# Kernel tuning notes

Hardware: AMD Instinct MI355X
Metric: run time of the kernel (lower is better)

Reference implementation:

```python
import jax, jax.numpy as jnp
import numpy as np


def _rotate_half(t):
    h = t.shape[-1] // 2
    return jnp.concatenate([-t[..., h:], t[..., :h]], axis=-1)


def setup_inputs() -> dict:
    key = jax.random.key(0)
    ks = jax.random.split(key, 4)
    B, S, H, NH, NKV, HD, MT = 1, 2048, 4096, 32, 8, 128, 8192
    x = jax.random.normal(ks[0], (B, S, H), jnp.float32)
    # real RoPE tables (HF rotate_half convention): [S, head_dim]
    inv_freq = 1.0 / (10000.0 ** (jnp.arange(0, HD, 2, dtype=jnp.float32) / HD))
    freqs = jnp.arange(S, dtype=jnp.float32)[:, None] * inv_freq[None, :]
    emb = jnp.concatenate([freqs, freqs], axis=-1)
    cos, sin = jnp.cos(emb), jnp.sin(emb)
    wq = jax.random.normal(ks[1], (H, H), jnp.float32) * 0.02
    w_kv = jax.random.normal(ks[2], (2 * NKV * HD, H), jnp.float32) * 0.02
    wo = jax.random.normal(ks[3], (H, H), jnp.float32) * 0.02
    cur_select_index = jnp.arange(B * S, dtype=jnp.int32)  # token slots in cache
    kv_buffer = jnp.zeros((MT, 2 * NKV, HD), jnp.float32)
    return dict(x=x, cos=cos, sin=sin, wq=wq, w_kv=w_kv, wo=wo,
                cur_select_index=cur_select_index, kv_buffer=kv_buffer)


def reference(x, cos, sin, wq, w_kv, wo, cur_select_index, kv_buffer):
    B, S, H = x.shape
    HD = cos.shape[-1]
    NKV = w_kv.shape[0] // (2 * HD)
    NH = H // HD
    # fused QKV projections
    q = (x @ wq.T).reshape(B, S, NH, HD)
    kvp = x @ w_kv.T  # [B, S, 2*NKV*HD]
    k = kvp[..., : NKV * HD].reshape(B, S, NKV, HD)
    v = kvp[..., NKV * HD:].reshape(B, S, NKV, HD)
    # RoPE (rotate_half), cos/sin broadcast over batch and heads
    c = cos[None, :, None, :]
    s = sin[None, :, None, :]
    q = q * c + _rotate_half(q) * s
    k = k * c + _rotate_half(k) * s
    # scatter KV-cache update: [B*S, 2*NKV, HD] into flat token cache
    combined_kv = jnp.concatenate([k, v], axis=2).reshape(B * S, 2 * NKV, HD)
    kv_new = kv_buffer.at[cur_select_index].set(combined_kv)
    # GQA: replicate kv heads to match query heads
    rep = NH // NKV
    kr = jnp.repeat(k, rep, axis=2)  # [B, S, NH, HD]
    vr = jnp.repeat(v, rep, axis=2)
    scale = 1.0 / jnp.sqrt(jnp.float32(HD))
    scores = jnp.einsum('bqhd,bkhd->bhqk', q, kr) * scale  # [B, NH, S, S]
    causal = jnp.tril(jnp.ones((S, S), dtype=bool))
    scores = jnp.where(causal[None, None], scores, jnp.float32(-1e9))
    p = jax.nn.softmax(scores, axis=-1)
    attn = jnp.einsum('bhqk,bkhd->bqhd', p, vr).reshape(B, S, H)
    out = attn @ wo.T
    return out, kv_new
```

## Files before the change

### kernel.cpp

```cpp
#include <hip/hip_runtime.h>
#include <stdint.h>
#include <stddef.h>

typedef __attribute__((ext_vector_type(8))) short bf16x8;
typedef __attribute__((ext_vector_type(4))) float f32x4;
typedef unsigned short u16;
typedef unsigned int u32;

static __device__ __forceinline__ u16 f2bf(float f) {
    u32 u = __builtin_bit_cast(u32, f);
    u = u + 0x7FFFu + ((u >> 16) & 1u);
    return (u16)(u >> 16);
}
static __device__ __forceinline__ float bf2f(u16 h) {
    return __builtin_bit_cast(float, (u32)h << 16);
}

typedef const __attribute__((address_space(1))) u32* gas1_t;
typedef __attribute__((address_space(3))) u32* las3_t;
static __device__ __forceinline__ void gload_lds16(const void* g, void* l) {
    __builtin_amdgcn_global_load_lds((gas1_t)g, (las3_t)l, 16, 0, 0);
}

__global__ __launch_bounds__(256) void k_cvt(const float* __restrict__ s,
                                             u16* __restrict__ d, int n) {
    int i = (blockIdx.x * 256 + threadIdx.x) * 4;
    if (i >= n) return;
    float4 f = *(const float4*)(s + i);
    ushort4 o;
    o.x = f2bf(f.x); o.y = f2bf(f.y); o.z = f2bf(f.z); o.w = f2bf(f.w);
    *(ushort4*)(d + i) = o;
}

template <bool F32OUT>
__global__ __launch_bounds__(256) void k_gemm_bt(const u16* __restrict__ A,
                                                 const u16* __restrict__ B,
                                                 void* __restrict__ Cv,
                                                 int M, int N, int K) {
    __shared__ alignas(16) unsigned char sA[16384];
    __shared__ alignas(16) unsigned char sB[16384];
    const int tid = threadIdx.x;
    const int lane = tid & 63;
    const int wid = tid >> 6;
    const int l15 = lane & 15, l4 = lane >> 4;
    const int brow = blockIdx.y * 128;
    const int bcol = blockIdx.x * 128;
    const int wr = wid >> 1, wc = wid & 1;

    f32x4 acc[4][4];
#pragma unroll
    for (int m = 0; m < 4; ++m)
#pragma unroll
        for (int n = 0; n < 4; ++n) acc[m][n] = (f32x4){0.f, 0.f, 0.f, 0.f};

    const int pbase = wid * 4096 + lane * 16;
    const int nk = K >> 6;
    for (int kt = 0; kt < nk; ++kt) {
        __syncthreads();
#pragma unroll
        for (int i = 0; i < 4; ++i) {
            const int p = pbase + i * 1024;
            const int row = p >> 7;
            const int colb = (p & 127) ^ ((row & 7) << 4);
            const char* gA = (const char*)(A + (size_t)(brow + row) * K + (kt << 6)) + colb;
            const char* gB = (const char*)(B + (size_t)(bcol + row) * K + (kt << 6)) + colb;
            gload_lds16(gA, sA + wid * 4096 + i * 1024);
            gload_lds16(gB, sB + wid * 4096 + i * 1024);
        }
        __syncthreads();
#pragma unroll
        for (int kk = 0; kk < 2; ++kk) {
            bf16x8 af[4], bfr[4];
#pragma unroll
            for (int m = 0; m < 4; ++m) {
                const int row = wr * 64 + m * 16 + l15;
                const int colb = (kk * 64 + l4 * 16) ^ ((row & 7) << 4);
                af[m] = *(const bf16x8*)(sA + row * 128 + colb);
            }
#pragma unroll
            for (int n = 0; n < 4; ++n) {
                const int row = wc * 64 + n * 16 + l15;
                const int colb = (kk * 64 + l4 * 16) ^ ((row & 7) << 4);
                bfr[n] = *(const bf16x8*)(sB + row * 128 + colb);
            }
#pragma unroll
            for (int m = 0; m < 4; ++m)
#pragma unroll
                for (int n = 0; n < 4; ++n)
                    acc[m][n] = __builtin_amdgcn_mfma_f32_16x16x32_bf16(
                        af[m], bfr[n], acc[m][n], 0, 0, 0);
        }
    }
#pragma unroll
    for (int m = 0; m < 4; ++m)
#pragma unroll
        for (int n = 0; n < 4; ++n)
#pragma unroll
            for (int q = 0; q < 4; ++q) {
                const int row = brow + wr * 64 + m * 16 + l4 * 4 + q;
                const int col = bcol + wc * 64 + n * 16 + l15;
                if constexpr (F32OUT)
                    ((float*)Cv)[(size_t)row * N + col] = acc[m][n][q];
                else
                    ((u16*)Cv)[(size_t)row * N + col] = f2bf(acc[m][n][q]);
            }
}

__global__ __launch_bounds__(256) void k_rope(u16* __restrict__ q,
                                              u16* __restrict__ kv,
                                              const float* __restrict__ cosb,
                                              const float* __restrict__ sinb) {
    int i = blockIdx.x * 256 + threadIdx.x;
    int s = i / 2560;
    int rem = i - s * 2560;
    int hh = rem >> 6;
    int d = rem & 63;
    float c = cosb[s * 128 + d];
    float sn = sinb[s * 128 + d];
    u16* p = (hh < 32) ? (q + (size_t)s * 4096 + hh * 128 + d)
                       : (kv + (size_t)s * 2048 + (hh - 32) * 128 + d);
    float a = bf2f(p[0]);
    float b = bf2f(p[64]);
    p[0]  = f2bf(a * c - b * sn);
    p[64] = f2bf(b * c + a * sn);
}

__global__ __launch_bounds__(256) void k_scatter(const u16* __restrict__ kv,
                                                 const int* __restrict__ sel,
                                                 float* __restrict__ kvnew) {
    int i = blockIdx.x * 256 + threadIdx.x;
    int row = i >> 9;
    int c4 = (i & 511) << 2;
    int r = sel[row];
    ushort4 v = *(const ushort4*)(kv + (size_t)row * 2048 + c4);
    float4 f;
    f.x = bf2f(v.x); f.y = bf2f(v.y); f.z = bf2f(v.z); f.w = bf2f(v.w);
    *(float4*)(kvnew + (size_t)r * 2048 + c4) = f;
}

__global__ __launch_bounds__(256) void k_attn(const u16* __restrict__ Q,
                                              const u16* __restrict__ KV,
                                              u16* __restrict__ Oa, int S) {
    __shared__ alignas(16) unsigned char sQ[16384];
    __shared__ alignas(16) unsigned char sK[16384];
    __shared__ alignas(16) unsigned char sV[16384];
    __shared__ alignas(16) unsigned char sP[4 * 16 * 160];
    const int tid = threadIdx.x;
    const int lane = tid & 63;
    const int w = tid >> 6;
    const int l15 = lane & 15, l4 = lane >> 4;
    const int h = blockIdx.x;
    const int q0 = blockIdx.y * 64;
    const int hk = h >> 2;

    {
        const int pb = w * 4096 + lane * 16;
#pragma unroll
        for (int i = 0; i < 4; ++i) {
            const int p = pb + i * 1024;
            const int row = p >> 8;
            const int colb = (p & 255) ^ ((row & 7) << 4);
            const char* g = (const char*)(Q + (size_t)(q0 + row) * 4096 + h * 128) + colb;
            gload_lds16(g, sQ + w * 4096 + i * 1024);
        }
    }
    __syncthreads();
    bf16x8 qf[4];
    {
        const int row = w * 16 + l15;
#pragma unroll
        for (int kk = 0; kk < 4; ++kk) {
            const int colb = (kk * 64 + l4 * 16) ^ ((row & 7) << 4);
            qf[kk] = *(const bf16x8*)(sQ + row * 256 + colb);
        }
    }
    float mrow[4] = {-1e30f, -1e30f, -1e30f, -1e30f};
    float lrow[4] = {0.f, 0.f, 0.f, 0.f};
    f32x4 oacc[8];
#pragma unroll
    for (int dn = 0; dn < 8; ++dn) oacc[dn] = (f32x4){0.f, 0.f, 0.f, 0.f};

    const float scale = 0.08838834764831845f;
    const int ntiles = (q0 >> 6) + 1;
    for (int t = 0; t < ntiles; ++t) {
        const int kv0 = t << 6;
        __syncthreads();
        {
            const int pb = w * 4096 + lane * 16;
#pragma unroll
            for (int i = 0; i < 4; ++i) {
                const int p = pb + i * 1024;
                const int row = p >> 8;
                const int colb = (p & 255) ^ ((row & 7) << 4);
                const char* gk = (const char*)(KV + (size_t)(kv0 + row) * 2048 + hk * 128) + colb;
                const char* gv = (const char*)(KV + (size_t)(kv0 + row) * 2048 + 1024 + hk * 128) + colb;
                gload_lds16(gk, sK + w * 4096 + i * 1024);
                gload_lds16(gv, sV + w * 4096 + i * 1024);
            }
        }
        __syncthreads();
        f32x4 sf[4];
#pragma unroll
        for (int n = 0; n < 4; ++n) {
            sf[n] = (f32x4){0.f, 0.f, 0.f, 0.f};
#pragma unroll
            for (int kk = 0; kk < 4; ++kk) {
                const int row = n * 16 + l15;
                const int colb = (kk * 64 + l4 * 16) ^ ((row & 7) << 4);
                bf16x8 kf = *(const bf16x8*)(sK + row * 256 + colb);
                sf[n] = __builtin_amdgcn_mfma_f32_16x16x32_bf16(qf[kk], kf, sf[n], 0, 0, 0);
            }
        }
        const bool diag = (kv0 == q0);
#pragma unroll
        for (int n = 0; n < 4; ++n)
#pragma unroll
            for (int q = 0; q < 4; ++q) {
                float v = sf[n][q] * scale;
                if (diag) {
                    const int col = n * 16 + l15;
                    const int rowq = w * 16 + l4 * 4 + q;
                    if (col > rowq) v = -1e9f;
                }
                sf[n][q] = v;
            }
        float al[4], rsum[4];
#pragma unroll
        for (int q = 0; q < 4; ++q) {
            float m0 = fmaxf(fmaxf(sf[0][q], sf[1][q]), fmaxf(sf[2][q], sf[3][q]));
#pragma unroll
            for (int d = 1; d < 16; d <<= 1) m0 = fmaxf(m0, __shfl_xor(m0, d));
            const float mn = fmaxf(mrow[q], m0);
            al[q] = __expf(mrow[q] - mn);
            mrow[q] = mn;
            rsum[q] = 0.f;
        }
#pragma unroll
        for (int n = 0; n < 4; ++n)
#pragma unroll
            for (int q = 0; q < 4; ++q) {
                float p = __expf(sf[n][q] - mrow[q]);
                sf[n][q] = p;
                rsum[q] += p;
            }
#pragma unroll
        for (int q = 0; q < 4; ++q) {
#pragma unroll
            for (int d = 1; d < 16; d <<= 1) rsum[q] += __shfl_xor(rsum[q], d);
            lrow[q] = lrow[q] * al[q] + rsum[q];
        }
#pragma unroll
        for (int dn = 0; dn < 8; ++dn) {
            oacc[dn][0] *= al[0]; oacc[dn][1] *= al[1];
            oacc[dn][2] *= al[2]; oacc[dn][3] *= al[3];
        }
        {
            u16* pw = (u16*)(sP + w * 2560);
#pragma unroll
            for (int n = 0; n < 4; ++n)
#pragma unroll
                for (int q = 0; q < 4; ++q)
                    pw[(l4 * 4 + q) * 80 + n * 16 + l15] = f2bf(sf[n][q]);
        }
#pragma unroll
        for (int kk2 = 0; kk2 < 2; ++kk2) {
            bf16x8 pf = *(const bf16x8*)(sP + w * 2560 + l15 * 160 + kk2 * 64 + l4 * 16);
#pragma unroll
            for (int dn = 0; dn < 8; ++dn) {
                bf16x8 vf;
#pragma unroll
                for (int j = 0; j < 8; ++j) {
                    const int k = kk2 * 32 + l4 * 8 + j;
                    const int byteoff = k * 256 + ((dn * 32 + l15 * 2) ^ ((k & 7) << 4));
                    vf[j] = (short)*(const u16*)(sV + byteoff);
                }
                oacc[dn] = __builtin_amdgcn_mfma_f32_16x16x32_bf16(pf, vf, oacc[dn], 0, 0, 0);
            }
        }
    }
#pragma unroll
    for (int dn = 0; dn < 8; ++dn)
#pragma unroll
        for (int q = 0; q < 4; ++q) {
            const int row = q0 + w * 16 + l4 * 4 + q;
            const int col = h * 128 + dn * 16 + l15;
            Oa[(size_t)row * 4096 + col] = f2bf(oacc[dn][q] / lrow[q]);
        }
}

extern "C" void kernel_launch(void* const* d_in, const int* in_sizes, int n_in,
                              void* d_out, int out_size, void* d_ws, size_t ws_size,
                              hipStream_t stream) {
    (void)n_in; (void)out_size; (void)ws_size;
    const float* x    = (const float*)d_in[0];
    const float* cosb = (const float*)d_in[1];
    const float* sinb = (const float*)d_in[2];
    const float* wq   = (const float*)d_in[3];
    const float* wkv  = (const float*)d_in[4];
    const float* wo   = (const float*)d_in[5];
    const int*   sel  = (const int*)d_in[6];
    const float* kvbuf = (const float*)d_in[7];

    const int H = 4096, HKV = 2048;
    const int S = in_sizes[0] / H;
    const int MT = in_sizes[7] / HKV;

    char* ws = (char*)d_ws;
    u16* xb    = (u16*)(ws);
    u16* attnb = (u16*)(ws);
    u16* wqb   = (u16*)(ws + (16u << 20));
    u16* wob   = (u16*)(ws + (16u << 20));
    u16* wkvb  = (u16*)(ws + (48u << 20));
    u16* qb    = (u16*)(ws + (64u << 20));
    u16* kvb   = (u16*)(ws + (80u << 20));

    float* out = (float*)d_out;
    float* kvnew = out + (size_t)S * H;

    const int nx = S * H, nwq = H * H, nwkv = HKV * H, nwo = H * H;
    k_cvt<<<nx / 1024, 256, 0, stream>>>(x, xb, nx);
    k_cvt<<<nwq / 1024, 256, 0, stream>>>(wq, wqb, nwq);
    k_cvt<<<nwkv / 1024, 256, 0, stream>>>(wkv, wkvb, nwkv);

    k_gemm_bt<false><<<dim3(H / 128, S / 128), 256, 0, stream>>>(xb, wqb, qb, S, H, H);
    k_gemm_bt<false><<<dim3(HKV / 128, S / 128), 256, 0, stream>>>(xb, wkvb, kvb, S, HKV, H);

    k_cvt<<<nwo / 1024, 256, 0, stream>>>(wo, wob, nwo);

    k_rope<<<(S * 2560) / 256, 256, 0, stream>>>(qb, kvb, cosb, sinb);

    hipMemcpyAsync(kvnew, kvbuf, (size_t)MT * HKV * sizeof(float),
                   hipMemcpyDeviceToDevice, stream);
    k_scatter<<<(S * HKV / 4) / 256, 256, 0, stream>>>(kvb, sel, kvnew);

    k_attn<<<dim3(32, S / 64), 256, 0, stream>>>(qb, kvb, attnb, S);

    k_gemm_bt<true><<<dim3(H / 128, S / 128), 256, 0, stream>>>(attnb, wob, out, S, H, H);
}
```

Measured before the change: 716.2 us.

## Transpose V into LDS through registers for vectorized PV operand reads

V tiles are now loaded into registers, transposed with 16-bit pack/shift operations, and stored to LDS in a d-major swizzled layout. The PV MFMA B operand then comes from a single 16-byte LDS read instead of eight scalar u16 reads. The P staging buffer now reuses the Q shared buffer, since Q lives in registers after the prologue. The cost is that V no longer uses async direct-to-LDS loads: it takes synchronous global loads plus register shuffling each tile, which can stall before the barrier.

```diff
diff --git a/kernel.cpp b/kernel.cpp
--- a/kernel.cpp
+++ b/kernel.cpp
@@ -141,10 +141,9 @@
 __global__ __launch_bounds__(256) void k_attn(const u16* __restrict__ Q,
                                               const u16* __restrict__ KV,
                                               u16* __restrict__ Oa, int S) {
-    __shared__ alignas(16) unsigned char sQ[16384];
+    __shared__ alignas(16) unsigned char sQP[16384];
     __shared__ alignas(16) unsigned char sK[16384];
     __shared__ alignas(16) unsigned char sV[16384];
-    __shared__ alignas(16) unsigned char sP[4 * 16 * 160];
     const int tid = threadIdx.x;
     const int lane = tid & 63;
     const int w = tid >> 6;
@@ -161,7 +160,7 @@
             const int row = p >> 8;
             const int colb = (p & 255) ^ ((row & 7) << 4);
             const char* g = (const char*)(Q + (size_t)(q0 + row) * 4096 + h * 128) + colb;
-            gload_lds16(g, sQ + w * 4096 + i * 1024);
+            gload_lds16(g, sQP + w * 4096 + i * 1024);
         }
     }
     __syncthreads();
@@ -171,7 +170,7 @@
 #pragma unroll
         for (int kk = 0; kk < 4; ++kk) {
             const int colb = (kk * 64 + l4 * 16) ^ ((row & 7) << 4);
-            qf[kk] = *(const bf16x8*)(sQ + row * 256 + colb);
+            qf[kk] = *(const bf16x8*)(sQP + row * 256 + colb);
         }
     }
     float mrow[4] = {-1e30f, -1e30f, -1e30f, -1e30f};
@@ -179,12 +178,23 @@
     f32x4 oacc[8];
 #pragma unroll
     for (int dn = 0; dn < 8; ++dn) oacc[dn] = (f32x4){0.f, 0.f, 0.f, 0.f};
+
+    const int vko = (tid & 7) * 8;
+    const int vdq = (tid >> 3) * 4;
 
     const float scale = 0.08838834764831845f;
     const int ntiles = (q0 >> 6) + 1;
     for (int t = 0; t < ntiles; ++t) {
         const int kv0 = t << 6;
         __syncthreads();
+        u32 vin[8][2];
+#pragma unroll
+        for (int i = 0; i < 8; ++i) {
+            const u32* g = (const u32*)(KV + (size_t)(kv0 + vko + i) * 2048 +
+                                        1024 + hk * 128 + vdq);
+            vin[i][0] = g[0];
+            vin[i][1] = g[1];
+        }
         {
             const int pb = w * 4096 + lane * 16;
 #pragma unroll
@@ -193,10 +203,33 @@
                 const int row = p >> 8;
                 const int colb = (p & 255) ^ ((row & 7) << 4);
                 const char* gk = (const char*)(KV + (size_t)(kv0 + row) * 2048 + hk * 128) + colb;
-                const char* gv = (const char*)(KV + (size_t)(kv0 + row) * 2048 + 1024 + hk * 128) + colb;
                 gload_lds16(gk, sK + w * 4096 + i * 1024);
-                gload_lds16(gv, sV + w * 4096 + i * 1024);
-            }
+            }
+        }
+#pragma unroll
+        for (int q = 0; q < 4; ++q) {
+            const int d = vdq + q;
+            uint4 ow;
+            {
+                const int wsel = q >> 1;
+                u32 a0 = vin[0][wsel], b0 = vin[1][wsel];
+                u32 a1 = vin[2][wsel], b1 = vin[3][wsel];
+                u32 a2 = vin[4][wsel], b2 = vin[5][wsel];
+                u32 a3 = vin[6][wsel], b3 = vin[7][wsel];
+                if (q & 1) {
+                    ow.x = (a0 >> 16) | (b0 & 0xFFFF0000u);
+                    ow.y = (a1 >> 16) | (b1 & 0xFFFF0000u);
+                    ow.z = (a2 >> 16) | (b2 & 0xFFFF0000u);
+                    ow.w = (a3 >> 16) | (b3 & 0xFFFF0000u);
+                } else {
+                    ow.x = (a0 & 0xFFFFu) | (b0 << 16);
+                    ow.y = (a1 & 0xFFFFu) | (b1 << 16);
+                    ow.z = (a2 & 0xFFFFu) | (b2 << 16);
+                    ow.w = (a3 & 0xFFFFu) | (b3 << 16);
+                }
+            }
+            const int byteoff = d * 128 + ((vko * 2) ^ ((d & 7) << 4));
+            *(uint4*)(sV + byteoff) = ow;
         }
         __syncthreads();
         f32x4 sf[4];
@@ -255,7 +288,7 @@
             oacc[dn][2] *= al[2]; oacc[dn][3] *= al[3];
         }
         {
-            u16* pw = (u16*)(sP + w * 2560);
+            u16* pw = (u16*)(sQP + w * 2560);
 #pragma unroll
             for (int n = 0; n < 4; ++n)
 #pragma unroll
@@ -264,16 +297,12 @@
         }
 #pragma unroll
         for (int kk2 = 0; kk2 < 2; ++kk2) {
-            bf16x8 pf = *(const bf16x8*)(sP + w * 2560 + l15 * 160 + kk2 * 64 + l4 * 16);
+            bf16x8 pf = *(const bf16x8*)(sQP + w * 2560 + l15 * 160 + kk2 * 64 + l4 * 16);
 #pragma unroll
             for (int dn = 0; dn < 8; ++dn) {
-                bf16x8 vf;
-#pragma unroll
-                for (int j = 0; j < 8; ++j) {
-                    const int k = kk2 * 32 + l4 * 8 + j;
-                    const int byteoff = k * 256 + ((dn * 32 + l15 * 2) ^ ((k & 7) << 4));
-                    vf[j] = (short)*(const u16*)(sV + byteoff);
-                }
+                const int d = dn * 16 + l15;
+                bf16x8 vf = *(const bf16x8*)(sV + d * 128 +
+                                             ((kk2 * 64 + l4 * 16) ^ ((d & 7) << 4)));
                 oacc[dn] = __builtin_amdgcn_mfma_f32_16x16x32_bf16(pf, vf, oacc[dn], 0, 0, 0);
             }
         }
```

After: 717.7 us. No clear change (+0.2%).
